# Kernel tuning notes

Hardware: AMD Instinct MI355X
Metric: run time of the kernel (lower is better)

Reference implementation:

```python
import jax, jax.numpy as jnp
import numpy as np
from jax import lax


def _binarize(t):
    # sign binarization to +1/-1 (zero maps to -1, matching torch.where(t > 0, 1, -1))
    return jnp.where(t > 0, 1.0, -1.0).astype(t.dtype)


def _bconv(x, w, b):
    # binary conv: binarize input and weights, then standard 3x3 'same' conv
    y = lax.conv_general_dilated(
        _binarize(x), _binarize(w),
        window_strides=(1, 1), padding=((1, 1), (1, 1)),
        dimension_numbers=('NCHW', 'OIHW', 'NCHW'))
    return y + b[None, :, None, None]


def _maxpool2(x):
    return lax.reduce_window(x, -jnp.inf, lax.max, (1, 1, 2, 2), (1, 1, 2, 2), 'VALID')


def setup_inputs() -> dict:
    key = jax.random.key(0)
    ks = jax.random.split(key, 13)
    s = 0.1
    return {
        'x': jax.random.normal(ks[0], (4096, 1, 28, 28), jnp.float32),
        'w1': jax.random.normal(ks[1], (32, 1, 3, 3), jnp.float32) * s,
        'b1': jax.random.normal(ks[2], (32,), jnp.float32) * s,
        'w2': jax.random.normal(ks[3], (64, 32, 3, 3), jnp.float32) * s,
        'b2': jax.random.normal(ks[4], (64,), jnp.float32) * s,
        'w3': jax.random.normal(ks[5], (16, 64, 3, 3), jnp.float32) * s,
        'b3': jax.random.normal(ks[6], (16,), jnp.float32) * s,
        'fc1_w': jax.random.normal(ks[7], (256, 16 * 7 * 7), jnp.float32) * s,
        'fc1_b': jax.random.normal(ks[8], (256,), jnp.float32) * s,
        'fc2_w': jax.random.normal(ks[9], (128, 256), jnp.float32) * s,
        'fc2_b': jax.random.normal(ks[10], (128,), jnp.float32) * s,
        'fc3_w': jax.random.normal(ks[11], (10, 128), jnp.float32) * s,
        'fc3_b': jax.random.normal(ks[12], (10,), jnp.float32) * s,
    }


def reference(x, w1, b1, w2, b2, w3, b3, fc1_w, fc1_b, fc2_w, fc2_b, fc3_w, fc3_b):
    h = jax.nn.relu(_maxpool2(_bconv(x, w1, b1)))      # [B,32,14,14]
    h = jax.nn.relu(_maxpool2(_bconv(h, w2, b2)))      # [B,64,7,7]
    h = jax.nn.relu(_bconv(h, w3, b3))                 # [B,16,7,7]
    h = h.reshape(-1, 16 * 7 * 7)
    h = jax.nn.relu(h @ fc1_w.T + fc1_b)
    h = jax.nn.relu(h @ fc2_w.T + fc2_b)
    return h @ fc3_w.T + fc3_b                          # [B,10]
```

## Files before the change

### kernel.cpp

```cpp
#include <hip/hip_runtime.h>
#include <cstdint>

#define OFF_W1T   4096
#define OFF_W2T   823296
#define OFF_H3T   954368
#define OFF_H1T   14061568
#define OFF_H2T   18255872

#define TW_WB1    0
#define TW_W2     32
#define TW_W3     608
#define TW_CORR2  896
#define TW_CORR3  1920
#define TW_TLE1   2176
#define TW_TGE1   2208
#define TW_TLE2   2240
#define TW_TGE2   2304

__device__ __forceinline__ int imin2(int a, int b) { return a < b ? a : b; }
__device__ __forceinline__ int imax2(int a, int b) { return a > b ? a : b; }

__device__ __forceinline__ void gload16(const float* g, float* lbase, int lane) {
#if __has_builtin(__builtin_amdgcn_global_load_lds)
    __builtin_amdgcn_global_load_lds(
        (const __attribute__((address_space(1))) uint32_t*)g,
        (__attribute__((address_space(3))) uint32_t*)lbase, 16, 0, 0);
#else
    *(float4*)&lbase[lane * 4] = *(const float4*)g;
#endif
}

__global__ __launch_bounds__(256) void prep(
    const float* __restrict__ w1, const float* __restrict__ b1,
    const float* __restrict__ w2, const float* __restrict__ b2,
    const float* __restrict__ w3,
    const float* __restrict__ fc1_w, const float* __restrict__ fc2_w,
    int* __restrict__ tab, float* __restrict__ w1T, float* __restrict__ w2T) {
    int t = threadIdx.x;
    uint32_t* utab = (uint32_t*)tab;
    if (blockIdx.x == 0) {
        if (t < 32) {
            uint32_t b = 0;
            for (int k = 0; k < 9; ++k) b |= (w1[t * 9 + k] > 0.f ? 1u : 0u) << k;
            utab[TW_WB1 + t] = b;
            tab[TW_TLE1 + t] = (int)floorf((9.f + b1[t]) * 0.5f);
            tab[TW_TGE1 + t] = (int)floorf(-b1[t]) + 1;
        }
        if (t >= 32 && t < 96) {
            int oc = t - 32;
            tab[TW_TLE2 + oc] = (int)floorf((288.f + b2[oc]) * 0.5f);
            tab[TW_TGE2 + oc] = (int)floorf(-b2[oc]) + 1;
        }
        for (int idx = t; idx < 576; idx += 256) {
            int oc = idx / 9, tap = idx % 9;
            int kh = tap / 3, kw = tap % 3;
            uint32_t b = 0;
            for (int ic = 0; ic < 32; ++ic)
                b |= (w2[((oc * 32 + ic) * 3 + kh) * 3 + kw] > 0.f ? 1u : 0u) << ic;
            utab[TW_W2 + idx] = b;
        }
        for (int idx = t; idx < 288; idx += 256) {
            int oc = idx / 18, rem = idx % 18;
            int tap = rem >> 1, word = rem & 1;
            int kh = tap / 3, kw = tap % 3;
            uint32_t b = 0;
            for (int ic = 0; ic < 32; ++ic)
                b |= (w3[((oc * 64 + ic + 32 * word) * 3 + kh) * 3 + kw] > 0.f ? 1u : 0u) << ic;
            utab[TW_W3 + idx] = b;
        }
        __syncthreads();
        for (int idx = t; idx < 1024; idx += 256) {
            int pat = idx >> 6, oc = idx & 63;
            int s = 0, n = 0;
            for (int tap = 0; tap < 9; ++tap) {
                int kh = tap / 3, kw = tap % 3;
                bool pad = ((pat & 1) && kh == 0) || ((pat & 2) && kh == 2) ||
                           ((pat & 4) && kw == 0) || ((pat & 8) && kw == 2);
                if (pad) { s += __popc(utab[TW_W2 + oc * 9 + tap]); ++n; }
            }
            tab[TW_CORR2 + idx] = 2 * s - 32 * n;
        }
        {
            int idx = t;
            if (idx < 256) {
                int pat = idx >> 4, oc = idx & 15;
                int s = 0, n = 0;
                for (int tap = 0; tap < 9; ++tap) {
                    int kh = tap / 3, kw = tap % 3;
                    bool pad = ((pat & 1) && kh == 0) || ((pat & 2) && kh == 2) ||
                               ((pat & 4) && kw == 0) || ((pat & 8) && kw == 2);
                    if (pad) {
                        s += __popc(utab[TW_W3 + oc * 18 + tap * 2]) +
                             __popc(utab[TW_W3 + oc * 18 + tap * 2 + 1]);
                        ++n;
                    }
                }
                tab[TW_CORR3 + idx] = 2 * s - 64 * n;
            }
        }
    } else {
        int e = (blockIdx.x - 1) * 256 + t;
        if (e < 204800) {
            int k = e >> 8, n = e & 255;
            w1T[e] = (k < 784) ? fc1_w[n * 784 + k] : 0.f;
        } else {
            int e2 = e - 204800;
            int k = e2 >> 7, n = e2 & 127;
            w2T[e2] = fc2_w[n * 256 + k];
        }
    }
}

#define WV 456

__global__ __launch_bounds__(512, 8) void conv_stack(
    const float* __restrict__ x,
    const float* __restrict__ b3,
    const int* __restrict__ tab,
    float* __restrict__ h3T,
    int imgbase) {
    __shared__ int SH[1280 + 4 * WV];
    const int t = threadIdx.x;
    const int wid = t >> 6, lane = t & 63;
    const int iml = wid >> 1, sw = wid & 1;
    const int img = imgbase + blockIdx.x * 4 + iml;
    const uint32_t* utab = (const uint32_t*)tab;
    uint32_t* W = (uint32_t*)&SH[1280 + iml * WV];

    for (int i = t; i < 1280; i += 512) SH[i] = tab[TW_CORR2 + i];
    for (int i = t; i < 4 * WV; i += 512) SH[1280 + i] = 0;
    __syncthreads();

    if (lane < 14) {
        int r = sw * 14 + lane;
        const float* xr = x + img * 784 + r * 28;
        uint32_t b = 0;
#pragma unroll
        for (int q = 0; q < 7; ++q) {
            float4 v = *(const float4*)(xr + q * 4);
            b |= (v.x > 0.f ? 1u : 0u) << (q * 4 + 0);
            b |= (v.y > 0.f ? 1u : 0u) << (q * 4 + 1);
            b |= (v.z > 0.f ? 1u : 0u) << (q * 4 + 2);
            b |= (v.w > 0.f ? 1u : 0u) << (q * 4 + 3);
        }
        W[1 + r] = b << 1;
    }
    __syncthreads();

    auto conv1_int = [&](int p) {
        int Pi = 1 + p / 12, Pj = 1 + p % 12;
        int i0 = 2 * Pi, j0 = 2 * Pj;
        uint32_t r0 = W[i0], r1 = W[i0 + 1], r2 = W[i0 + 2], r3 = W[i0 + 3];
        uint32_t f0a = (r0 >> j0) & 7, f0b = (r0 >> (j0 + 1)) & 7;
        uint32_t f1a = (r1 >> j0) & 7, f1b = (r1 >> (j0 + 1)) & 7;
        uint32_t f2a = (r2 >> j0) & 7, f2b = (r2 >> (j0 + 1)) & 7;
        uint32_t f3a = (r3 >> j0) & 7, f3b = (r3 >> (j0 + 1)) & 7;
        uint32_t s00 = f0a | (f1a << 3) | (f2a << 6);
        uint32_t s01 = f0b | (f1b << 3) | (f2b << 6);
        uint32_t s10 = f1a | (f2a << 3) | (f3a << 6);
        uint32_t s11 = f1b | (f2b << 3) | (f3b << 6);
        uint32_t word = 0;
#pragma unroll
        for (int oc = 0; oc < 32; ++oc) {
            uint32_t w = utab[TW_WB1 + oc];
            int m0 = __popc(s00 ^ w), m1 = __popc(s01 ^ w);
            int m2 = __popc(s10 ^ w), m3 = __popc(s11 ^ w);
            int mn = imin2(imin2(m0, m1), imin2(m2, m3));
            word |= (mn <= tab[TW_TLE1 + oc] ? 1u : 0u) << oc;
        }
        W[32 + (Pi + 1) * 16 + (Pj + 1)] = word;
    };
    if (sw == 0) {
        conv1_int(lane);
        conv1_int(64 + lane);
    } else {
        if (lane < 16) conv1_int(128 + lane);
        int p = lane;
        bool act = p < 52;
        int pp = act ? p : 28;
        int Pi, Pj;
        if (pp < 14)      { Pi = 0;  Pj = pp; }
        else if (pp < 28) { Pi = 13; Pj = pp - 14; }
        else if (pp < 40) { Pi = pp - 28 + 1; Pj = 0; }
        else              { Pi = pp - 40 + 1; Pj = 13; }
        int i0 = 2 * Pi, j0 = 2 * Pj;
        uint32_t r0 = W[i0], r1 = W[i0 + 1], r2 = W[i0 + 2], r3 = W[i0 + 3];
        uint32_t f0a = (r0 >> j0) & 7, f0b = (r0 >> (j0 + 1)) & 7;
        uint32_t f1a = (r1 >> j0) & 7, f1b = (r1 >> (j0 + 1)) & 7;
        uint32_t f2a = (r2 >> j0) & 7, f2b = (r2 >> (j0 + 1)) & 7;
        uint32_t f3a = (r3 >> j0) & 7, f3b = (r3 >> (j0 + 1)) & 7;
        uint32_t smp[4];
        smp[0] = f0a | (f1a << 3) | (f2a << 6);
        smp[1] = f0b | (f1b << 3) | (f2b << 6);
        smp[2] = f1a | (f2a << 3) | (f3a << 6);
        smp[3] = f1b | (f2b << 3) | (f3b << 6);
        uint32_t mb[4];
        int pcm[4];
#pragma unroll
        for (int a = 0; a < 2; ++a) {
            int i = 2 * Pi + a;
            uint32_t vre = 0x1FF;
            if (i == 0)  vre &= ~0x007u;
            if (i == 27) vre &= ~0x1C0u;
#pragma unroll
            for (int bb = 0; bb < 2; ++bb) {
                int j = 2 * Pj + bb;
                uint32_t vce = 0x1FF;
                if (j == 0)  vce &= ~0x049u;
                if (j == 27) vce &= ~0x124u;
                mb[a * 2 + bb] = vre & vce;
                pcm[a * 2 + bb] = __popc(vre & vce);
            }
        }
        uint32_t word = 0;
#pragma unroll
        for (int oc = 0; oc < 32; ++oc) {
            uint32_t w = utab[TW_WB1 + oc];
            int best = -1000;
#pragma unroll
            for (int p4 = 0; p4 < 4; ++p4) {
                int v = pcm[p4] - 2 * __popc((smp[p4] ^ w) & mb[p4]);
                best = imax2(best, v);
            }
            word |= (best >= tab[TW_TGE1 + oc] ? 1u : 0u) << oc;
        }
        if (act) W[32 + (Pi + 1) * 16 + (Pj + 1)] = word;
    }
    __syncthreads();

    {
        uint32_t w2r[9];
#pragma unroll
        for (int k = 0; k < 9; ++k) w2r[k] = utab[TW_W2 + lane * 9 + k];
        const int tle2 = tab[TW_TLE2 + lane];
        const int tge2 = tab[TW_TGE2 + lane];
        const uint32_t* H1 = W + 32;
        uint32_t* H2 = W + 288;

        for (int q = sw; q < 25; q += 2) {
            int Pi = 1 + q / 5, Pj = 1 + q % 5;
            uint32_t c[16];
#pragma unroll
            for (int r = 0; r < 4; ++r) {
                uint2 lo = *(const uint2*)&H1[(2 * Pi + r) * 16 + 2 * Pj];
                uint2 hi = *(const uint2*)&H1[(2 * Pi + r) * 16 + 2 * Pj + 2];
                c[r * 4 + 0] = lo.x; c[r * 4 + 1] = lo.y;
                c[r * 4 + 2] = hi.x; c[r * 4 + 3] = hi.y;
            }
            int mn = 100000;
#pragma unroll
            for (int a = 0; a < 2; ++a)
#pragma unroll
                for (int bb = 0; bb < 2; ++bb) {
                    int s = 0;
#pragma unroll
                    for (int kh = 0; kh < 3; ++kh)
#pragma unroll
                        for (int kw = 0; kw < 3; ++kw)
                            s += __popc(c[(a + kh) * 4 + (bb + kw)] ^ w2r[kh * 3 + kw]);
                    mn = imin2(mn, s);
                }
            uint64_t bal = __ballot(mn <= tle2);
            if (lane == 0) {
                uint2 wv = make_uint2((uint32_t)bal, (uint32_t)(bal >> 32));
                *(uint2*)&H2[((Pi + 1) * 9 + (Pj + 1)) * 2] = wv;
            }
        }
        for (int bp = sw; bp < 24; bp += 2) {
            int Pi, Pj;
            if (bp < 7)       { Pi = 0; Pj = bp; }
            else if (bp < 14) { Pi = 6; Pj = bp - 7; }
            else if (bp < 19) { Pi = bp - 14 + 1; Pj = 0; }
            else              { Pi = bp - 19 + 1; Pj = 6; }
            uint32_t c[16];
#pragma unroll
            for (int r = 0; r < 4; ++r) {
                uint2 lo = *(const uint2*)&H1[(2 * Pi + r) * 16 + 2 * Pj];
                uint2 hi = *(const uint2*)&H1[(2 * Pi + r) * 16 + 2 * Pj + 2];
                c[r * 4 + 0] = lo.x; c[r * 4 + 1] = lo.y;
                c[r * 4 + 2] = hi.x; c[r * 4 + 3] = hi.y;
            }
            int best = -100000;
#pragma unroll
            for (int a = 0; a < 2; ++a)
#pragma unroll
                for (int bb = 0; bb < 2; ++bb) {
                    int s = 0;
#pragma unroll
                    for (int kh = 0; kh < 3; ++kh)
#pragma unroll
                        for (int kw = 0; kw < 3; ++kw)
                            s += __popc(c[(a + kh) * 4 + (bb + kw)] ^ w2r[kh * 3 + kw]);
                    int i = 2 * Pi + a, j = 2 * Pj + bb;
                    int pat = (i == 0 ? 1 : 0) | (i == 13 ? 2 : 0) |
                              (j == 0 ? 4 : 0) | (j == 13 ? 8 : 0);
                    int D = 288 - 2 * s + SH[pat * 64 + lane];
                    best = imax2(best, D);
                }
            uint64_t bal = __ballot(best >= tge2);
            if (lane == 0) {
                uint2 wv = make_uint2((uint32_t)bal, (uint32_t)(bal >> 32));
                *(uint2*)&H2[((Pi + 1) * 9 + (Pj + 1)) * 2] = wv;
            }
        }
    }
    __syncthreads();

    {
        const uint32_t* H2 = (const uint32_t*)W + 288;
        int oc = lane & 15, sub = lane >> 4;
        uint32_t w3r[18];
#pragma unroll
        for (int k = 0; k < 18; ++k) w3r[k] = utab[TW_W3 + oc * 18 + k];
        float bias3 = b3[oc];
        const int gbeg = sw ? 6 : 0, gend = sw ? 13 : 6;
        for (int g = gbeg; g < gend; ++g) {
            int pos = g * 4 + sub;
            bool act = pos < 49;
            int pp = act ? pos : 0;
            int Pi = pp / 7, Pj = pp % 7;
            int s = 0;
#pragma unroll
            for (int kh = 0; kh < 3; ++kh)
#pragma unroll
                for (int kw = 0; kw < 3; ++kw) {
                    uint2 hv = *(const uint2*)&H2[((Pi + kh) * 9 + (Pj + kw)) * 2];
                    s += __popc(hv.x ^ w3r[(kh * 3 + kw) * 2]) +
                         __popc(hv.y ^ w3r[(kh * 3 + kw) * 2 + 1]);
                }
            int pat = (Pi == 0 ? 1 : 0) | (Pi == 6 ? 2 : 0) |
                      (Pj == 0 ? 4 : 0) | (Pj == 6 ? 8 : 0);
            int D = 576 - 2 * s + SH[1024 + pat * 16 + oc];
            float h = (float)D + bias3;
            h = h > 0.f ? h : 0.f;
            if (act) h3T[(oc * 49 + pp) * 4096 + img] = h;
        }
    }
}

__global__ __launch_bounds__(256) void fc1_gemm(
    const float* __restrict__ aT,
    const float* __restrict__ bT,
    const float* __restrict__ bias,
    float* __restrict__ oT) {
    const int KC = 40;
    __shared__ float As[2][KC * 64];
    __shared__ float Bs[2][KC * 64];
    const int t = threadIdx.x;
    const int lane = t & 63, wid = t >> 6;
    const int tx = t & 15, ty = t >> 4;
    const int img0 = blockIdx.x * 64;
    const int n0 = blockIdx.y * 64;
    float acc[4][4] = {{0.f}};

    auto stage = [&](int buf, int kc) {
        for (int s = wid; s < 20; s += 4) {
            int seg = s < 10 ? s : s - 10;
            int kk = seg * 4 + (lane >> 4);
            int c = (lane & 15) * 4;
            if (s < 10)
                gload16(&aT[(kc + kk) * 4096 + img0 + c], &As[buf][seg * 256], lane);
            else
                gload16(&bT[(kc + kk) * 256 + n0 + c], &Bs[buf][seg * 256], lane);
        }
    };

    stage(0, 0);
    asm volatile("s_waitcnt vmcnt(0)" ::: "memory");
    __builtin_amdgcn_s_barrier();
    for (int ch = 0; ch < 20; ++ch) {
        int buf = ch & 1;
        if (ch < 19) {
            stage(buf ^ 1, (ch + 1) * KC);
            asm volatile("s_waitcnt vmcnt(5)" ::: "memory");
        } else {
            asm volatile("s_waitcnt vmcnt(0)" ::: "memory");
        }
        __builtin_amdgcn_s_barrier();
        const float* A = As[buf];
        const float* B = Bs[buf];
#pragma unroll 8
        for (int kk = 0; kk < KC; ++kk) {
            float4 a = *(const float4*)&A[kk * 64 + ty * 4];
            float4 b = *(const float4*)&B[kk * 64 + tx * 4];
            acc[0][0] += a.x * b.x; acc[0][1] += a.x * b.y;
            acc[0][2] += a.x * b.z; acc[0][3] += a.x * b.w;
            acc[1][0] += a.y * b.x; acc[1][1] += a.y * b.y;
            acc[1][2] += a.y * b.z; acc[1][3] += a.y * b.w;
            acc[2][0] += a.z * b.x; acc[2][1] += a.z * b.y;
            acc[2][2] += a.z * b.z; acc[2][3] += a.z * b.w;
            acc[3][0] += a.w * b.x; acc[3][1] += a.w * b.y;
            acc[3][2] += a.w * b.z; acc[3][3] += a.w * b.w;
        }
        __builtin_amdgcn_s_barrier();
    }
    float4 bb = *(const float4*)&bias[n0 + tx * 4];
    float bv[4] = {bb.x, bb.y, bb.z, bb.w};
#pragma unroll
    for (int jj = 0; jj < 4; ++jj) {
        float4 ov;
        ov.x = acc[0][jj] + bv[jj]; ov.x = ov.x > 0.f ? ov.x : 0.f;
        ov.y = acc[1][jj] + bv[jj]; ov.y = ov.y > 0.f ? ov.y : 0.f;
        ov.z = acc[2][jj] + bv[jj]; ov.z = ov.z > 0.f ? ov.z : 0.f;
        ov.w = acc[3][jj] + bv[jj]; ov.w = ov.w > 0.f ? ov.w : 0.f;
        *(float4*)&oT[(n0 + tx * 4 + jj) * 4096 + img0 + ty * 4] = ov;
    }
}

__global__ __launch_bounds__(256) void fc2_gemm(
    const float* __restrict__ aT,
    const float* __restrict__ bT,
    const float* __restrict__ bias,
    float* __restrict__ oT) {
    const int KC = 64;
    __shared__ float As[2][KC * 64];
    __shared__ float Bs[2][KC * 32];
    const int t = threadIdx.x;
    const int lane = t & 63, wid = t >> 6;
    const int tx = t & 15, ty = t >> 4;
    const int img0 = blockIdx.x * 64;
    const int n0 = blockIdx.y * 32;
    float acc[4][2] = {{0.f}};

    auto stage = [&](int buf, int kc) {
        for (int s = wid; s < 24; s += 4) {
            if (s < 16) {
                int kk = s * 4 + (lane >> 4);
                int c = (lane & 15) * 4;
                gload16(&aT[(kc + kk) * 4096 + img0 + c], &As[buf][s * 256], lane);
            } else {
                int seg = s - 16;
                int kk = seg * 8 + (lane >> 3);
                int c = (lane & 7) * 4;
                gload16(&bT[(kc + kk) * 128 + n0 + c], &Bs[buf][seg * 256], lane);
            }
        }
    };

    stage(0, 0);
    asm volatile("s_waitcnt vmcnt(0)" ::: "memory");
    __builtin_amdgcn_s_barrier();
    for (int ch = 0; ch < 4; ++ch) {
        int buf = ch & 1;
        if (ch < 3) {
            stage(buf ^ 1, (ch + 1) * KC);
            asm volatile("s_waitcnt vmcnt(6)" ::: "memory");
        } else {
            asm volatile("s_waitcnt vmcnt(0)" ::: "memory");
        }
        __builtin_amdgcn_s_barrier();
        const float* A = As[buf];
        const float* B = Bs[buf];
#pragma unroll 8
        for (int kk = 0; kk < KC; ++kk) {
            float4 a = *(const float4*)&A[kk * 64 + ty * 4];
            float2 b = *(const float2*)&B[kk * 32 + tx * 2];
            acc[0][0] += a.x * b.x; acc[0][1] += a.x * b.y;
            acc[1][0] += a.y * b.x; acc[1][1] += a.y * b.y;
            acc[2][0] += a.z * b.x; acc[2][1] += a.z * b.y;
            acc[3][0] += a.w * b.x; acc[3][1] += a.w * b.y;
        }
        __builtin_amdgcn_s_barrier();
    }
#pragma unroll
    for (int j = 0; j < 2; ++j) {
        int n = n0 + tx * 2 + j;
        float bj = bias[n];
        float4 ov;
        ov.x = acc[0][j] + bj; ov.x = ov.x > 0.f ? ov.x : 0.f;
        ov.y = acc[1][j] + bj; ov.y = ov.y > 0.f ? ov.y : 0.f;
        ov.z = acc[2][j] + bj; ov.z = ov.z > 0.f ? ov.z : 0.f;
        ov.w = acc[3][j] + bj; ov.w = ov.w > 0.f ? ov.w : 0.f;
        *(float4*)&oT[n * 4096 + img0 + ty * 4] = ov;
    }
}

__global__ __launch_bounds__(256) void fc3_gemm(
    const float* __restrict__ aT,
    const float* __restrict__ w,
    const float* __restrict__ bias,
    float* __restrict__ out) {
    int id = blockIdx.x * 256 + threadIdx.x;
    int n = id >> 12, img = id & 4095;
    const float* wr = w + n * 128;
    float a0 = 0.f, a1 = 0.f, a2 = 0.f, a3 = 0.f;
#pragma unroll 8
    for (int k = 0; k < 128; k += 4) {
        a0 += aT[(k + 0) * 4096 + img] * wr[k + 0];
        a1 += aT[(k + 1) * 4096 + img] * wr[k + 1];
        a2 += aT[(k + 2) * 4096 + img] * wr[k + 2];
        a3 += aT[(k + 3) * 4096 + img] * wr[k + 3];
    }
    out[img * 10 + n] = (a0 + a1) + (a2 + a3) + bias[n];
}

extern "C" void kernel_launch(void* const* d_in, const int* in_sizes, int n_in,
                              void* d_out, int out_size, void* d_ws, size_t ws_size,
                              hipStream_t stream) {
    const float* x     = (const float*)d_in[0];
    const float* w1    = (const float*)d_in[1];
    const float* b1    = (const float*)d_in[2];
    const float* w2    = (const float*)d_in[3];
    const float* b2    = (const float*)d_in[4];
    const float* w3    = (const float*)d_in[5];
    const float* b3    = (const float*)d_in[6];
    const float* fc1_w = (const float*)d_in[7];
    const float* fc1_b = (const float*)d_in[8];
    const float* fc2_w = (const float*)d_in[9];
    const float* fc2_b = (const float*)d_in[10];
    const float* fc3_w = (const float*)d_in[11];
    const float* fc3_b = (const float*)d_in[12];
    float* out = (float*)d_out;

    const int B = in_sizes[0] / 784;
    char* ws = (char*)d_ws;
    float* w1T = (float*)(ws + OFF_W1T);
    float* w2T = (float*)(ws + OFF_W2T);
    float* h3T = (float*)(ws + OFF_H3T);
    float* h1T = (float*)(ws + OFF_H1T);
    float* h2T = (float*)(ws + OFF_H2T);
    int* tab = (int*)(ws + OFF_H2T);

    hipLaunchKernelGGL(prep, dim3(929), dim3(256), 0, stream,
                       w1, b1, w2, b2, w3, fc1_w, fc2_w, tab, w1T, w2T);
    hipLaunchKernelGGL(conv_stack, dim3(B / 8), dim3(512), 0, stream,
                       x, b3, tab, h3T, 0);
    hipLaunchKernelGGL(conv_stack, dim3(B / 8), dim3(512), 0, stream,
                       x, b3, tab, h3T, B / 2);
    hipLaunchKernelGGL(fc1_gemm, dim3(B / 64, 4), dim3(256), 0, stream,
                       h3T, w1T, fc1_b, h1T);
    hipLaunchKernelGGL(fc2_gemm, dim3(B / 64, 4), dim3(256), 0, stream,
                       h1T, w2T, fc2_b, h2T);
    hipLaunchKernelGGL(fc3_gemm, dim3(B * 10 / 256), dim3(256), 0, stream,
                       h2T, fc3_w, fc3_b, out);
}
```

Baseline: 235.2 us.

## Tile weight transposes through LDS, merge conv launches, narrow fc1 N-tiles

The prep kernel now transposes fc1 and fc2 weights in 64x64 tiles through padded shared memory, so both reads and writes are coalesced. This replaces the per-element strided gather and cuts the prep grid from 929 blocks to 61. The two half-batch conv_stack launches are merged into one launch over the whole batch, removing a launch and its tail. fc1_gemm now uses 32-wide N tiles with twice as many blocks, trading more A-tile reloads for better occupancy and a smaller per-thread register tile.

```diff
diff --git a/kernel.cpp b/kernel.cpp
--- a/kernel.cpp
+++ b/kernel.cpp
@@ -80,33 +80,56 @@
             }
             tab[TW_CORR2 + idx] = 2 * s - 32 * n;
         }
-        {
-            int idx = t;
-            if (idx < 256) {
-                int pat = idx >> 4, oc = idx & 15;
-                int s = 0, n = 0;
-                for (int tap = 0; tap < 9; ++tap) {
-                    int kh = tap / 3, kw = tap % 3;
-                    bool pad = ((pat & 1) && kh == 0) || ((pat & 2) && kh == 2) ||
-                               ((pat & 4) && kw == 0) || ((pat & 8) && kw == 2);
-                    if (pad) {
-                        s += __popc(utab[TW_W3 + oc * 18 + tap * 2]) +
-                             __popc(utab[TW_W3 + oc * 18 + tap * 2 + 1]);
-                        ++n;
-                    }
+        if (t < 256) {
+            int pat = t >> 4, oc = t & 15;
+            int s = 0, n = 0;
+            for (int tap = 0; tap < 9; ++tap) {
+                int kh = tap / 3, kw = tap % 3;
+                bool pad = ((pat & 1) && kh == 0) || ((pat & 2) && kh == 2) ||
+                           ((pat & 4) && kw == 0) || ((pat & 8) && kw == 2);
+                if (pad) {
+                    s += __popc(utab[TW_W3 + oc * 18 + tap * 2]) +
+                         __popc(utab[TW_W3 + oc * 18 + tap * 2 + 1]);
+                    ++n;
                 }
-                tab[TW_CORR3 + idx] = 2 * s - 64 * n;
-            }
+            }
+            tab[TW_CORR3 + t] = 2 * s - 64 * n;
+        }
+    } else if (blockIdx.x <= 52) {
+        __shared__ float T[64][65];
+        int bb = blockIdx.x - 1;
+        int kt = bb >> 2, nt = bb & 3;
+#pragma unroll
+        for (int s = 0; s < 16; ++s) {
+            int idx = s * 256 + t;
+            int nl = idx >> 6, kl = idx & 63;
+            int k = kt * 64 + kl;
+            T[nl][kl] = (k < 784) ? fc1_w[(nt * 64 + nl) * 784 + k] : 0.f;
+        }
+        __syncthreads();
+#pragma unroll
+        for (int s = 0; s < 16; ++s) {
+            int idx = s * 256 + t;
+            int kl = idx >> 6, nl = idx & 63;
+            int k = kt * 64 + kl;
+            if (k < 800) w1T[k * 256 + nt * 64 + nl] = T[nl][kl];
         }
     } else {
-        int e = (blockIdx.x - 1) * 256 + t;
-        if (e < 204800) {
-            int k = e >> 8, n = e & 255;
-            w1T[e] = (k < 784) ? fc1_w[n * 784 + k] : 0.f;
-        } else {
-            int e2 = e - 204800;
-            int k = e2 >> 7, n = e2 & 127;
-            w2T[e2] = fc2_w[n * 256 + k];
+        __shared__ float T[64][65];
+        int bb = blockIdx.x - 53;
+        int kt = bb >> 1, nt = bb & 1;
+#pragma unroll
+        for (int s = 0; s < 16; ++s) {
+            int idx = s * 256 + t;
+            int nl = idx >> 6, kl = idx & 63;
+            T[nl][kl] = fc2_w[(nt * 64 + nl) * 256 + kt * 64 + kl];
+        }
+        __syncthreads();
+#pragma unroll
+        for (int s = 0; s < 16; ++s) {
+            int idx = s * 256 + t;
+            int kl = idx >> 6, nl = idx & 63;
+            w2T[(kt * 64 + kl) * 128 + nt * 64 + nl] = T[nl][kl];
         }
     }
 }
@@ -117,13 +140,12 @@
     const float* __restrict__ x,
     const float* __restrict__ b3,
     const int* __restrict__ tab,
-    float* __restrict__ h3T,
-    int imgbase) {
+    float* __restrict__ h3T) {
     __shared__ int SH[1280 + 4 * WV];
     const int t = threadIdx.x;
     const int wid = t >> 6, lane = t & 63;
     const int iml = wid >> 1, sw = wid & 1;
-    const int img = imgbase + blockIdx.x * 4 + iml;
+    const int img = blockIdx.x * 4 + iml;
     const uint32_t* utab = (const uint32_t*)tab;
     uint32_t* W = (uint32_t*)&SH[1280 + iml * WV];
 
@@ -345,23 +367,26 @@
     float* __restrict__ oT) {
     const int KC = 40;
     __shared__ float As[2][KC * 64];
-    __shared__ float Bs[2][KC * 64];
+    __shared__ float Bs[2][KC * 32];
     const int t = threadIdx.x;
     const int lane = t & 63, wid = t >> 6;
     const int tx = t & 15, ty = t >> 4;
     const int img0 = blockIdx.x * 64;
-    const int n0 = blockIdx.y * 64;
-    float acc[4][4] = {{0.f}};
+    const int n0 = blockIdx.y * 32;
+    float acc[4][2] = {{0.f}};
 
     auto stage = [&](int buf, int kc) {
-        for (int s = wid; s < 20; s += 4) {
-            int seg = s < 10 ? s : s - 10;
-            int kk = seg * 4 + (lane >> 4);
-            int c = (lane & 15) * 4;
-            if (s < 10)
-                gload16(&aT[(kc + kk) * 4096 + img0 + c], &As[buf][seg * 256], lane);
-            else
+        for (int s = wid; s < 15; s += 4) {
+            if (s < 10) {
+                int kk = s * 4 + (lane >> 4);
+                int c = (lane & 15) * 4;
+                gload16(&aT[(kc + kk) * 4096 + img0 + c], &As[buf][s * 256], lane);
+            } else {
+                int seg = s - 10;
+                int kk = seg * 8 + (lane >> 3);
+                int c = (lane & 7) * 4;
                 gload16(&bT[(kc + kk) * 256 + n0 + c], &Bs[buf][seg * 256], lane);
+            }
         }
     };
 
@@ -372,7 +397,7 @@
         int buf = ch & 1;
         if (ch < 19) {
             stage(buf ^ 1, (ch + 1) * KC);
-            asm volatile("s_waitcnt vmcnt(5)" ::: "memory");
+            asm volatile("s_waitcnt vmcnt(3)" ::: "memory");
         } else {
             asm volatile("s_waitcnt vmcnt(0)" ::: "memory");
         }
@@ -382,28 +407,24 @@
 #pragma unroll 8
         for (int kk = 0; kk < KC; ++kk) {
             float4 a = *(const float4*)&A[kk * 64 + ty * 4];
-            float4 b = *(const float4*)&B[kk * 64 + tx * 4];
+            float2 b = *(const float2*)&B[kk * 32 + tx * 2];
             acc[0][0] += a.x * b.x; acc[0][1] += a.x * b.y;
-            acc[0][2] += a.x * b.z; acc[0][3] += a.x * b.w;
             acc[1][0] += a.y * b.x; acc[1][1] += a.y * b.y;
-            acc[1][2] += a.y * b.z; acc[1][3] += a.y * b.w;
             acc[2][0] += a.z * b.x; acc[2][1] += a.z * b.y;
-            acc[2][2] += a.z * b.z; acc[2][3] += a.z * b.w;
             acc[3][0] += a.w * b.x; acc[3][1] += a.w * b.y;
-            acc[3][2] += a.w * b.z; acc[3][3] += a.w * b.w;
         }
         __builtin_amdgcn_s_barrier();
     }
-    float4 bb = *(const float4*)&bias[n0 + tx * 4];
-    float bv[4] = {bb.x, bb.y, bb.z, bb.w};
-#pragma unroll
-    for (int jj = 0; jj < 4; ++jj) {
+#pragma unroll
+    for (int j = 0; j < 2; ++j) {
+        int n = n0 + tx * 2 + j;
+        float bj = bias[n];
         float4 ov;
-        ov.x = acc[0][jj] + bv[jj]; ov.x = ov.x > 0.f ? ov.x : 0.f;
-        ov.y = acc[1][jj] + bv[jj]; ov.y = ov.y > 0.f ? ov.y : 0.f;
-        ov.z = acc[2][jj] + bv[jj]; ov.z = ov.z > 0.f ? ov.z : 0.f;
-        ov.w = acc[3][jj] + bv[jj]; ov.w = ov.w > 0.f ? ov.w : 0.f;
-        *(float4*)&oT[(n0 + tx * 4 + jj) * 4096 + img0 + ty * 4] = ov;
+        ov.x = acc[0][j] + bj; ov.x = ov.x > 0.f ? ov.x : 0.f;
+        ov.y = acc[1][j] + bj; ov.y = ov.y > 0.f ? ov.y : 0.f;
+        ov.z = acc[2][j] + bj; ov.z = ov.z > 0.f ? ov.z : 0.f;
+        ov.w = acc[3][j] + bj; ov.w = ov.w > 0.f ? ov.w : 0.f;
+        *(float4*)&oT[n * 4096 + img0 + ty * 4] = ov;
     }
 }
 
@@ -521,13 +542,11 @@
     float* h2T = (float*)(ws + OFF_H2T);
     int* tab = (int*)(ws + OFF_H2T);
 
-    hipLaunchKernelGGL(prep, dim3(929), dim3(256), 0, stream,
+    hipLaunchKernelGGL(prep, dim3(61), dim3(256), 0, stream,
                        w1, b1, w2, b2, w3, fc1_w, fc2_w, tab, w1T, w2T);
-    hipLaunchKernelGGL(conv_stack, dim3(B / 8), dim3(512), 0, stream,
-                       x, b3, tab, h3T, 0);
-    hipLaunchKernelGGL(conv_stack, dim3(B / 8), dim3(512), 0, stream,
-                       x, b3, tab, h3T, B / 2);
-    hipLaunchKernelGGL(fc1_gemm, dim3(B / 64, 4), dim3(256), 0, stream,
+    hipLaunchKernelGGL(conv_stack, dim3(B / 4), dim3(512), 0, stream,
+                       x, b3, tab, h3T);
+    hipLaunchKernelGGL(fc1_gemm, dim3(B / 64, 8), dim3(256), 0, stream,
                        h3T, w1T, fc1_b, h1T);
     hipLaunchKernelGGL(fc2_gemm, dim3(B / 64, 4), dim3(256), 0, stream,
                        h1T, w2T, fc2_b, h2T);
```

New measurement: 215.4 us. -8.4%, faster.
